# Performance work log

Measured on AMD Instinct MI355X. Metric: run time of the kernel, lower is better.

Reference implementation:

```python
import jax, jax.numpy as jnp
import numpy as np

B, N, C, HEADS = 8, 1024, 768, 12
HW = 32  # H = W = 32, so H*W == N


def _layernorm(x, g, b, eps=1e-5):
    mu = x.mean(-1, keepdims=True)
    var = ((x - mu) ** 2).mean(-1, keepdims=True)
    return (x - mu) * jax.lax.rsqrt(var + eps) * g + b


def setup_inputs() -> dict:
    key = jax.random.key(0)
    ks = jax.random.split(key, 6)
    w = lambda k, shape: jax.random.normal(k, shape, dtype=jnp.float32) * 0.02
    return {
        "x": jax.random.normal(ks[0], (B, N, C), dtype=jnp.float32),
        "y": jax.random.normal(ks[1], (B, C, HW, HW), dtype=jnp.float32),
        "q_w": w(ks[2], (C, C)),
        "q_b": jnp.zeros((C,), jnp.float32),
        "kv_w": w(ks[3], (2 * C, C)),
        "kv_b": jnp.zeros((2 * C,), jnp.float32),
        "proj_w": w(ks[4], (C, C)),
        "proj_b": jnp.zeros((C,), jnp.float32),
        "ln_g": jnp.ones((C,), jnp.float32),
        "ln_b": jnp.zeros((C,), jnp.float32),
        "H": HW,
        "W": HW,
    }


def reference(x, y, q_w, q_b, kv_w, kv_b, proj_w, proj_b, ln_g, ln_b, H, W):
    Bn, Nn, Cn = x.shape
    hd = Cn // HEADS
    scale = hd ** -0.5  # qk_scale=None, c_ratio=1 -> head_dim**-0.5

    # gating tensors from y
    y1 = y.reshape(Bn, Cn, H * W).transpose(0, 2, 1)          # [B, N, C]
    y2 = _layernorm(y1, ln_g, ln_b)
    yq = jax.nn.sigmoid(y2 @ q_w.T + q_b)                      # [B, N, C]
    ykv = jax.nn.sigmoid(y2 @ kv_w.T + kv_b)                   # [B, N, 2C]

    # gated q: q2 = q0 + q0*yq
    q0 = x @ q_w.T + q_b
    q = (q0 + q0 * yq).reshape(Bn, Nn, HEADS, hd).transpose(0, 2, 1, 3)  # [B,h,N,d]

    # gated kv: kv2 = kv0*ykv + ykv
    kv0 = x @ kv_w.T + kv_b
    kv = (kv0 * ykv + ykv).reshape(Bn, Nn, 2, HEADS, hd).transpose(2, 0, 3, 1, 4)
    k, v = kv[0], kv[1]                                        # [B,h,N,d] each

    attn = jax.nn.softmax(jnp.einsum("bhqd,bhkd->bhqk", q, k) * scale, axis=-1)
    out = jnp.einsum("bhqk,bhkd->bhqd", attn, v)
    out = out.transpose(0, 2, 1, 3).reshape(Bn, Nn, Cn)
    return out @ proj_w.T + proj_b
```

## Files before the change

### kernel.cpp

```cpp
#include <hip/hip_runtime.h>
#include <stdint.h>

typedef __attribute__((ext_vector_type(4))) float f4;
typedef __attribute__((ext_vector_type(8))) short bf16x8;
typedef __attribute__((ext_vector_type(4))) unsigned short u16x4;
typedef unsigned short u16;

#define B_ 8
#define N_ 1024
#define C_ 768
#define NH 12
#define HD 64

__device__ __forceinline__ float bf2f(u16 v) {
  union { unsigned u; float f; } x; x.u = ((unsigned)v) << 16; return x.f;
}
__device__ __forceinline__ u16 f2bf(float f) {
  union { float f; unsigned u; } x; x.f = f;
  unsigned r = x.u + 0x7FFFu + ((x.u >> 16) & 1u);
  return (u16)(r >> 16);
}
__device__ __forceinline__ void g2l16(const u16* g, const u16* l) {
  __builtin_amdgcn_global_load_lds(
      (const __attribute__((address_space(1))) void*)(uintptr_t)g,
      (__attribute__((address_space(3))) void*)(uint32_t)(uintptr_t)l,
      16, 0, 0);
}

#define SW12() asm volatile("s_waitcnt vmcnt(12)" ::: "memory")
#define SW6()  asm volatile("s_waitcnt vmcnt(6)" ::: "memory")
#define SW4()  asm volatile("s_waitcnt vmcnt(4)" ::: "memory")
#define SW3()  asm volatile("s_waitcnt vmcnt(3)" ::: "memory")
#define SW2()  asm volatile("s_waitcnt vmcnt(2)" ::: "memory")
#define SW0()  asm volatile("s_waitcnt vmcnt(0)" ::: "memory")
#define BARF()                              \
  do {                                      \
    __builtin_amdgcn_s_barrier();           \
    asm volatile("" ::: "memory");          \
    __builtin_amdgcn_sched_barrier(0);      \
  } while (0)

__global__ __launch_bounds__(256) void cvt_bf16(const float* __restrict__ s,
                                                u16* __restrict__ d, int n4) {
  int i = blockIdx.x * 256 + threadIdx.x;
  int stride = gridDim.x * 256;
  for (; i < n4; i += stride) {
    float4 v = ((const float4*)s)[i];
    u16x4 o;
    o.x = f2bf(v.x); o.y = f2bf(v.y); o.z = f2bf(v.z); o.w = f2bf(v.w);
    ((u16x4*)d)[i] = o;
  }
}

__global__ __launch_bounds__(512) void ln_fused(const float* __restrict__ y,
                                                const float* __restrict__ lg,
                                                const float* __restrict__ lb,
                                                u16* __restrict__ y2c,
                                                int b0) {
  __shared__ u16 ybuf[768 * 33];
  __shared__ float ps[16][32], pq[16][32];
  __shared__ float smu[32], srs[32];
  int t = threadIdx.x;
  int nl = t & 31, ch = t >> 5;
  int idx0 = b0 * N_ + blockIdx.x * 32;
  int b = idx0 >> 10, nb_ = idx0 & 1023;
  const float* p = y + (size_t)b * C_ * N_ + nb_ + nl;
  float s = 0.f, q = 0.f;
  int c0 = ch * 48;
  for (int c = c0; c < c0 + 48; ++c) {
    float v = p[(size_t)c * N_];
    s += v; q += v * v;
    ybuf[c * 33 + nl] = f2bf(v);
  }
  ps[ch][nl] = s; pq[ch][nl] = q;
  __syncthreads();
  if (t < 32) {
    float ts = 0.f, tq = 0.f;
    for (int g = 0; g < 16; ++g) { ts += ps[g][t]; tq += pq[g][t]; }
    float m = ts * (1.f / C_);
    float var = tq * (1.f / C_) - m * m;
    smu[t] = m;
    srs[t] = rsqrtf(fmaxf(var, 0.f) + 1e-5f);
  }
  __syncthreads();
  int rn = t >> 4, cg = t & 15;
  float m = smu[rn], rr = srs[rn];
  int bl = b - b0;
  int n = nb_ + rn;
  u16* dst = y2c + ((size_t)bl * N_ + n) * C_ + cg * 48;
  for (int cc = 0; cc < 48; cc += 8) {
    int c = cg * 48 + cc;
    bf16x8 o;
    for (int j = 0; j < 8; ++j) {
      float v = bf2f(ybuf[(c + j) * 33 + rn]);
      o[j] = (short)f2bf((v - m) * rr * lg[c + j] + lb[c + j]);
    }
    *(bf16x8*)(dst + cc) = o;
  }
}

__global__ __launch_bounds__(256, 2) void gemm_gate(
    const u16* __restrict__ xbc, const u16* __restrict__ y2c,
    const u16* __restrict__ qwb, const u16* __restrict__ kvwb,
    const float* __restrict__ qb_, const float* __restrict__ kvb_,
    u16* __restrict__ o_q, u16* __restrict__ o_k, u16* __restrict__ o_vT) {
  __shared__ u16 smem[36864];
  int t = threadIdx.x, l = t & 63;
  int quad = l >> 4, l15 = l & 15;
  int w = t >> 6, wm = w & 1, wn = w >> 1;
  int m0l = blockIdx.x * 128;
  int n0l = blockIdx.y * 128;

  const u16* wp; const float* bp; int sel, h0;
  if (n0l < C_) {
    wp = qwb + (size_t)n0l * C_; bp = qb_ + n0l; sel = 0; h0 = n0l >> 6;
  } else {
    int nk = n0l - C_;
    wp = kvwb + (size_t)nk * C_; bp = kvb_ + nk;
    sel = (nk < C_) ? 1 : 2;
    h0 = ((sel == 2) ? nk - C_ : nk) >> 6;
  }

  f4 accx[4][4], accy[4][4];
  for (int i = 0; i < 4; ++i)
    for (int j = 0; j < 4; ++j) {
      accx[i][j] = (f4){0.f, 0.f, 0.f, 0.f};
      accy[i][j] = (f4){0.f, 0.f, 0.f, 0.f};
    }

  int row = t >> 2;
  int colS = (((t & 3) ^ (row & 3)) * 8);
  const u16* gx = xbc + (size_t)(m0l + row) * C_ + colS;
  const u16* gy = y2c + (size_t)(m0l + row) * C_ + colS;
  const u16* gw = wp + (size_t)row * C_ + colS;
  int rsl = (quad ^ (l15 & 3)) * 8;

#define STAGE_G(OFF, kk)                                   \
  do {                                                     \
    u16* p_ = smem + (OFF);                                \
    g2l16(gx + (kk),           p_ + t * 8);                \
    g2l16(gx + (kk) + 64 * C_, p_ + 2048 + t * 8);         \
    g2l16(gy + (kk),           p_ + 4096 + t * 8);         \
    g2l16(gy + (kk) + 64 * C_, p_ + 6144 + t * 8);         \
    g2l16(gw + (kk),           p_ + 8192 + t * 8);         \
    g2l16(gw + (kk) + 64 * C_, p_ + 10240 + t * 8);        \
  } while (0)

#define COMPUTE_G(OFF)                                                        \
  do {                                                                        \
    const u16* base = smem + (OFF);                                           \
    bf16x8 afx[4], afy[4], bfr[4];                                            \
    for (int i = 0; i < 4; ++i) {                                             \
      int ra = (wm * 64 + i * 16 + l15) * 32 + rsl;                           \
      afx[i] = *(const bf16x8*)&base[ra];                                     \
      afy[i] = *(const bf16x8*)&base[4096 + ra];                              \
      int rb = (wn * 64 + i * 16 + l15) * 32 + rsl;                           \
      bfr[i] = *(const bf16x8*)&base[8192 + rb];                              \
    }                                                                         \
    for (int i = 0; i < 4; ++i)                                               \
      for (int j = 0; j < 4; ++j) {                                           \
        accx[i][j] = __builtin_amdgcn_mfma_f32_16x16x32_bf16(afx[i], bfr[j], accx[i][j], 0, 0, 0); \
        accy[i][j] = __builtin_amdgcn_mfma_f32_16x16x32_bf16(afy[i], bfr[j], accy[i][j], 0, 0, 0); \
      }                                                                       \
  } while (0)

#define STEP_G(i, OFF)                                        \
  do {                                                        \
    COMPUTE_G(OFF);                                           \
    BARF();                                                   \
    if ((i) < 21)      { STAGE_G(OFF, ((i) + 3) * 32); SW12(); } \
    else if ((i) == 21) SW6();                                \
    else if ((i) == 22) SW0();                                \
    BARF();                                                   \
  } while (0)

  STAGE_G(0, 0);
  STAGE_G(12288, 32);
  STAGE_G(24576, 64);
  SW12();
  BARF();
#pragma unroll
  for (int n = 0; n < 24; n += 3) {
    STEP_G(n, 0);
    STEP_G(n + 1, 12288);
    STEP_G(n + 2, 24576);
  }
#undef STEP_G
#undef STAGE_G
#undef COMPUTE_G

  const int PITCH = 136;
  for (int j = 0; j < 4; ++j) {
    int cloc = wn * 64 + j * 16 + l15;
    float bias = bp[cloc];
    for (int i = 0; i < 4; ++i) {
      int rb0 = wm * 64 + i * 16 + quad * 4;
      for (int r = 0; r < 4; ++r) {
        int rloc = rb0 + r;
        float vx = accx[i][j][r] + bias;
        float vy = accy[i][j][r] + bias;
        float gg = 1.f / (1.f + __expf(-vy));
        float val = (sel == 0) ? vx * (1.f + gg) : gg * (vx + 1.f);
        u16 bv = f2bf(val);
        if (sel == 2) smem[cloc * PITCH + rloc] = bv;
        else          smem[rloc * PITCH + cloc] = bv;
      }
    }
  }
  __syncthreads();
  {
    int rr = t >> 1, hh = t & 1;
    const u16* src = smem + rr * PITCH + hh * 64;
    u16* dst;
    if (sel == 2) {
      int h = h0 + (rr >> 6), d = rr & 63;
      int bl = m0l >> 10, nbase = m0l & 1023;
      dst = o_vT + (size_t)((bl * NH + h) * HD + d) * N_ + nbase + hh * 64;
    } else {
      int gml = m0l + rr;
      int bl = gml >> 10, n = gml & 1023;
      int h = h0 + hh;
      dst = (sel == 0 ? o_q : o_k) + (size_t)((bl * NH + h) * N_ + n) * HD;
    }
    for (int c = 0; c < 8; ++c) {
      bf16x8 v = *(const bf16x8*)(src + c * 8);
      *(bf16x8*)(dst + c * 8) = v;
    }
  }
}

__global__ __launch_bounds__(512) void attn(const u16* __restrict__ qoc,
                                            const u16* __restrict__ koc,
                                            const u16* __restrict__ vTc,
                                            u16* __restrict__ aoc) {
  __shared__ u16 Qs[8192], Ks[8192], Vs[8192];
  __shared__ u16 Ps[128 * 72];
  int t = threadIdx.x, l = t & 63, w = t >> 6;
  int quad = l >> 4, l15 = l & 15;
  int bhl = blockIdx.y;
  int bl = bhl / NH, h = bhl % NH;
  int q0 = blockIdx.x * 128;
  int sr = t >> 3;
  int swo = ((t & 7) ^ (sr & 7)) * 8;
  const u16* qbp = qoc + ((size_t)bhl * N_ + q0) * HD;
  const u16* kb = koc + (size_t)bhl * N_ * HD;
  const u16* vb = vTc + (size_t)bhl * HD * N_;

#define STAGE_KV(OFF, key0)                                                \
  do {                                                                     \
    g2l16(kb + (size_t)((key0) + sr) * HD + swo, Ks + (OFF) + t * 8);      \
    g2l16(vb + (size_t)sr * N_ + (key0) + swo,   Vs + (OFF) + t * 8);      \
  } while (0)

  g2l16(qbp + (size_t)sr * HD + swo,        Qs + t * 8);
  g2l16(qbp + (size_t)(64 + sr) * HD + swo, Qs + 4096 + t * 8);
  STAGE_KV(0, 0);
  STAGE_KV(4096, 64);
  SW2();
  BARF();

  int sA = (quad ^ (l15 & 7)) * 8;
  int sB = sA ^ 32;
  bf16x8 aq0 = *(const bf16x8*)&Qs[(w * 16 + l15) * 64 + sA];
  bf16x8 aq1 = *(const bf16x8*)&Qs[(w * 16 + l15) * 64 + sB];
  f4 o[4];
  for (int i = 0; i < 4; ++i) o[i] = (f4){0.f, 0.f, 0.f, 0.f};
  f4 ls = (f4){0.f, 0.f, 0.f, 0.f};
  bf16x8 ones;
  for (int i = 0; i < 8; ++i) ones[i] = (short)0x3F80;

#define TILE_STEP(KOFF)                                                       \
  do {                                                                        \
    f4 s_[4];                                                                 \
    __builtin_amdgcn_s_setprio(1);                                            \
    for (int ni = 0; ni < 4; ++ni) {                                          \
      bf16x8 b0v = *(const bf16x8*)&Ks[(KOFF) + (ni * 16 + l15) * 64 + sA];   \
      bf16x8 b1v = *(const bf16x8*)&Ks[(KOFF) + (ni * 16 + l15) * 64 + sB];   \
      f4 z = (f4){0.f, 0.f, 0.f, 0.f};                                        \
      z = __builtin_amdgcn_mfma_f32_16x16x32_bf16(aq0, b0v, z, 0, 0, 0);      \
      z = __builtin_amdgcn_mfma_f32_16x16x32_bf16(aq1, b1v, z, 0, 0, 0);      \
      s_[ni] = z;                                                             \
    }                                                                         \
    __builtin_amdgcn_s_setprio(0);                                            \
    for (int ni = 0; ni < 4; ++ni)                                            \
      for (int r = 0; r < 4; ++r)                                             \
        Ps[(w * 16 + quad * 4 + r) * 72 + ni * 16 + l15] =                    \
            f2bf(__expf(s_[ni][r] * 0.125f));                                 \
    bf16x8 ap0 = *(const bf16x8*)&Ps[(w * 16 + l15) * 72 + quad * 8];         \
    bf16x8 ap1 = *(const bf16x8*)&Ps[(w * 16 + l15) * 72 + 32 + quad * 8];    \
    __builtin_amdgcn_s_setprio(1);                                            \
    for (int ni = 0; ni < 4; ++ni) {                                          \
      bf16x8 b0v = *(const bf16x8*)&Vs[(KOFF) + (ni * 16 + l15) * 64 + sA];   \
      bf16x8 b1v = *(const bf16x8*)&Vs[(KOFF) + (ni * 16 + l15) * 64 + sB];   \
      o[ni] = __builtin_amdgcn_mfma_f32_16x16x32_bf16(ap0, b0v, o[ni], 0, 0, 0); \
      o[ni] = __builtin_amdgcn_mfma_f32_16x16x32_bf16(ap1, b1v, o[ni], 0, 0, 0); \
    }                                                                         \
    ls = __builtin_amdgcn_mfma_f32_16x16x32_bf16(ap0, ones, ls, 0, 0, 0);     \
    ls = __builtin_amdgcn_mfma_f32_16x16x32_bf16(ap1, ones, ls, 0, 0, 0);     \
    __builtin_amdgcn_s_setprio(0);                                            \
  } while (0)

  for (int kt = 0; kt < 16; kt += 2) {
    TILE_STEP(0);
    BARF();
    if (kt + 2 < 16) { STAGE_KV(0, (kt + 2) * 64); SW2(); } else { SW0(); }
    BARF();
    TILE_STEP(4096);
    BARF();
    if (kt + 3 < 16) { STAGE_KV(4096, (kt + 3) * 64); SW2(); } else { SW0(); }
    BARF();
  }
#undef TILE_STEP
#undef STAGE_KV

  for (int ni = 0; ni < 4; ++ni)
    for (int r = 0; r < 4; ++r)
      Ps[(w * 16 + quad * 4 + r) * 72 + ni * 16 + l15] =
          f2bf(o[ni][r] / ls[r]);
  __syncthreads();
  {
    int rr = t >> 2, cc = t & 3;
    int n = q0 + rr;
    const u16* src = Ps + rr * 72 + cc * 16;
    u16* dst = aoc + ((size_t)bl * N_ + n) * C_ + h * HD + cc * 16;
    *(bf16x8*)dst = *(const bf16x8*)src;
    *(bf16x8*)(dst + 8) = *(const bf16x8*)(src + 8);
  }
}

__global__ __launch_bounds__(256, 2) void gemm_proj(const u16* __restrict__ aoc,
                                                    const u16* __restrict__ pwb,
                                                    const float* __restrict__ bias,
                                                    float* __restrict__ out,
                                                    int b0) {
  __shared__ u16 smem[24576];
  int t = threadIdx.x, l = t & 63;
  int quad = l >> 4, l15 = l & 15;
  int w = t >> 6, wm = w & 1, wn = w >> 1;
  int m0l = blockIdx.x * 128, n0 = blockIdx.y * 64;
  f4 acc[4][2];
  for (int i = 0; i < 4; ++i)
    for (int j = 0; j < 2; ++j) acc[i][j] = (f4){0.f, 0.f, 0.f, 0.f};
  int row = t >> 2, colb = (t & 3) * 8;
  const u16* ga = aoc + (size_t)(m0l + row) * C_ + colb;
  const u16* gw = pwb + (size_t)(n0 + row) * C_ + colb;

#define STAGE_P(OFF, kk)                                        \
  do {                                                          \
    u16* p_ = smem + (OFF);                                     \
    g2l16(ga + (kk),                p_ + t * 8);                \
    g2l16(ga + (kk) + 64 * C_,      p_ + 2048 + t * 8);         \
    g2l16(ga + (kk) + 32,           p_ + 4096 + t * 8);         \
    g2l16(ga + (kk) + 32 + 64 * C_, p_ + 6144 + t * 8);         \
    g2l16(gw + (kk),                p_ + 8192 + t * 8);         \
    g2l16(gw + (kk) + 32,           p_ + 10240 + t * 8);        \
  } while (0)

#define COMPUTE_P(OFF)                                                        \
  do {                                                                        \
    const u16* base = smem + (OFF);                                           \
    _Pragma("unroll")                                                         \
    for (int kh = 0; kh < 2; ++kh) {                                          \
      bf16x8 af[4], bfr[2];                                                   \
      for (int i = 0; i < 4; ++i)                                             \
        af[i] = *(const bf16x8*)&base[kh * 4096 + (wm * 64 + i * 16 + l15) * 32 + quad * 8]; \
      for (int j = 0; j < 2; ++j)                                             \
        bfr[j] = *(const bf16x8*)&base[8192 + kh * 2048 + (wn * 32 + j * 16 + l15) * 32 + quad * 8]; \
      for (int i = 0; i < 4; ++i)                                             \
        for (int j = 0; j < 2; ++j)                                           \
          acc[i][j] = __builtin_amdgcn_mfma_f32_16x16x32_bf16(af[i], bfr[j], acc[i][j], 0, 0, 0); \
    }                                                                         \
  } while (0)

  STAGE_P(0, 0);
  STAGE_P(12288, 64);
  SW6();
  BARF();
  for (int n = 0; n < 12; n += 2) {
    COMPUTE_P(0);
    BARF();
    if (n + 2 < 12) { STAGE_P(0, (n + 2) * 64); SW6(); } else { SW0(); }
    BARF();
    COMPUTE_P(12288);
    BARF();
    if (n + 3 < 12) { STAGE_P(12288, (n + 3) * 64); SW6(); } else { SW0(); }
    BARF();
  }
#undef STAGE_P
#undef COMPUTE_P

  for (int j = 0; j < 2; ++j) {
    int gcol = n0 + wn * 32 + j * 16 + l15;
    float bv = bias[gcol];
    for (int i = 0; i < 4; ++i) {
      int rbase = m0l + wm * 64 + i * 16 + quad * 4;
      for (int r = 0; r < 4; ++r)
        __builtin_nontemporal_store(acc[i][j][r] + bv,
                                    &out[(size_t)(b0 * N_ + rbase + r) * C_ + gcol]);
    }
  }
}

extern "C" void kernel_launch(void* const* d_in, const int* in_sizes, int n_in,
                              void* d_out, int out_size, void* d_ws, size_t ws_size,
                              hipStream_t stream) {
  const float* x   = (const float*)d_in[0];
  const float* y   = (const float*)d_in[1];
  const float* qw  = (const float*)d_in[2];
  const float* qb  = (const float*)d_in[3];
  const float* kvw = (const float*)d_in[4];
  const float* kvb = (const float*)d_in[5];
  const float* pw  = (const float*)d_in[6];
  const float* pb  = (const float*)d_in[7];
  const float* lg  = (const float*)d_in[8];
  const float* lb  = (const float*)d_in[9];

  char* ws = (char*)d_ws;
  u16* qwb  = (u16*)(ws + 65536);
  u16* kvwb = (u16*)(ws + 1245184);
  u16* pwb  = (u16*)(ws + 3604480);
  const size_t BASE2 = 4784128;
  const size_t PER_B = 1572864;

  int nb = 1;
  for (int c = 8; c >= 1; c >>= 1) {
    if (BASE2 + 5 * (size_t)c * PER_B <= ws_size) { nb = c; break; }
  }
  u16* xbc = (u16*)(ws + BASE2);
  u16* y2c = (u16*)(ws + BASE2 + (size_t)nb * PER_B);
  u16* qoc = (u16*)(ws + BASE2 + 2 * (size_t)nb * PER_B);
  u16* koc = (u16*)(ws + BASE2 + 3 * (size_t)nb * PER_B);
  u16* vTc = (u16*)(ws + BASE2 + 4 * (size_t)nb * PER_B);
  u16* aoc = xbc;

  cvt_bf16<<<dim3(576), dim3(256), 0, stream>>>(qw, qwb, 147456);
  cvt_bf16<<<dim3(1152), dim3(256), 0, stream>>>(kvw, kvwb, 294912);
  cvt_bf16<<<dim3(576), dim3(256), 0, stream>>>(pw, pwb, 147456);

  for (int b0 = 0; b0 < B_; b0 += nb) {
    cvt_bf16<<<dim3(768 * nb), dim3(256), 0, stream>>>(
        x + (size_t)b0 * N_ * C_, xbc, nb * 196608);
    ln_fused<<<dim3(32 * nb), dim3(512), 0, stream>>>(y, lg, lb, y2c, b0);
    gemm_gate<<<dim3(8 * nb, 18), dim3(256), 0, stream>>>(xbc, y2c, qwb, kvwb,
                                                          qb, kvb, qoc, koc, vTc);
    attn<<<dim3(8, 12 * nb), dim3(512), 0, stream>>>(qoc, koc, vTc, aoc);
    gemm_proj<<<dim3(8 * nb, 12), dim3(256), 0, stream>>>(aoc, pwb, pb, (float*)d_out, b0);
  }
}
```

Baseline: 268.2 us.

## Load K/V fragments directly from global memory, two query groups per wave

Replaces LDS-staged, double-buffered K/V tiles in the attention kernel with direct global-to-register fragment loads, and removes the block-wide barriers. Each wave now processes 32 query rows as two 16-row groups sharing each K/V fragment, and blocks shrink to 256 threads. This aims to cut LDS traffic and synchronisation overhead. In exchange, global loads are strided, less coalesced and not prefetched, so memory latency may be exposed.

```diff
diff --git a/kernel.cpp b/kernel.cpp
--- a/kernel.cpp
+++ b/kernel.cpp
@@ -29,9 +29,7 @@
 
 #define SW12() asm volatile("s_waitcnt vmcnt(12)" ::: "memory")
 #define SW6()  asm volatile("s_waitcnt vmcnt(6)" ::: "memory")
-#define SW4()  asm volatile("s_waitcnt vmcnt(4)" ::: "memory")
 #define SW3()  asm volatile("s_waitcnt vmcnt(3)" ::: "memory")
-#define SW2()  asm volatile("s_waitcnt vmcnt(2)" ::: "memory")
 #define SW0()  asm volatile("s_waitcnt vmcnt(0)" ::: "memory")
 #define BARF()                              \
   do {                                      \
@@ -229,102 +227,87 @@
   }
 }
 
-__global__ __launch_bounds__(512) void attn(const u16* __restrict__ qoc,
+__global__ __launch_bounds__(256) void attn(const u16* __restrict__ qoc,
                                             const u16* __restrict__ koc,
                                             const u16* __restrict__ vTc,
                                             u16* __restrict__ aoc) {
-  __shared__ u16 Qs[8192], Ks[8192], Vs[8192];
   __shared__ u16 Ps[128 * 72];
   int t = threadIdx.x, l = t & 63, w = t >> 6;
   int quad = l >> 4, l15 = l & 15;
   int bhl = blockIdx.y;
   int bl = bhl / NH, h = bhl % NH;
   int q0 = blockIdx.x * 128;
-  int sr = t >> 3;
-  int swo = ((t & 7) ^ (sr & 7)) * 8;
   const u16* qbp = qoc + ((size_t)bhl * N_ + q0) * HD;
   const u16* kb = koc + (size_t)bhl * N_ * HD;
   const u16* vb = vTc + (size_t)bhl * HD * N_;
 
-#define STAGE_KV(OFF, key0)                                                \
-  do {                                                                     \
-    g2l16(kb + (size_t)((key0) + sr) * HD + swo, Ks + (OFF) + t * 8);      \
-    g2l16(vb + (size_t)sr * N_ + (key0) + swo,   Vs + (OFF) + t * 8);      \
-  } while (0)
-
-  g2l16(qbp + (size_t)sr * HD + swo,        Qs + t * 8);
-  g2l16(qbp + (size_t)(64 + sr) * HD + swo, Qs + 4096 + t * 8);
-  STAGE_KV(0, 0);
-  STAGE_KV(4096, 64);
-  SW2();
-  BARF();
-
-  int sA = (quad ^ (l15 & 7)) * 8;
-  int sB = sA ^ 32;
-  bf16x8 aq0 = *(const bf16x8*)&Qs[(w * 16 + l15) * 64 + sA];
-  bf16x8 aq1 = *(const bf16x8*)&Qs[(w * 16 + l15) * 64 + sB];
-  f4 o[4];
-  for (int i = 0; i < 4; ++i) o[i] = (f4){0.f, 0.f, 0.f, 0.f};
-  f4 ls = (f4){0.f, 0.f, 0.f, 0.f};
+  bf16x8 aq[2][2];
+  for (int g = 0; g < 2; ++g) {
+    const u16* qrow = qbp + (size_t)(w * 32 + g * 16 + l15) * HD;
+    aq[g][0] = *(const bf16x8*)(qrow + quad * 8);
+    aq[g][1] = *(const bf16x8*)(qrow + 32 + quad * 8);
+  }
+
+  f4 o[2][4]; f4 ls[2];
+  for (int g = 0; g < 2; ++g) {
+    ls[g] = (f4){0.f, 0.f, 0.f, 0.f};
+    for (int i = 0; i < 4; ++i) o[g][i] = (f4){0.f, 0.f, 0.f, 0.f};
+  }
   bf16x8 ones;
   for (int i = 0; i < 8; ++i) ones[i] = (short)0x3F80;
 
-#define TILE_STEP(KOFF)                                                       \
-  do {                                                                        \
-    f4 s_[4];                                                                 \
-    __builtin_amdgcn_s_setprio(1);                                            \
-    for (int ni = 0; ni < 4; ++ni) {                                          \
-      bf16x8 b0v = *(const bf16x8*)&Ks[(KOFF) + (ni * 16 + l15) * 64 + sA];   \
-      bf16x8 b1v = *(const bf16x8*)&Ks[(KOFF) + (ni * 16 + l15) * 64 + sB];   \
-      f4 z = (f4){0.f, 0.f, 0.f, 0.f};                                        \
-      z = __builtin_amdgcn_mfma_f32_16x16x32_bf16(aq0, b0v, z, 0, 0, 0);      \
-      z = __builtin_amdgcn_mfma_f32_16x16x32_bf16(aq1, b1v, z, 0, 0, 0);      \
-      s_[ni] = z;                                                             \
-    }                                                                         \
-    __builtin_amdgcn_s_setprio(0);                                            \
-    for (int ni = 0; ni < 4; ++ni)                                            \
-      for (int r = 0; r < 4; ++r)                                             \
-        Ps[(w * 16 + quad * 4 + r) * 72 + ni * 16 + l15] =                    \
-            f2bf(__expf(s_[ni][r] * 0.125f));                                 \
-    bf16x8 ap0 = *(const bf16x8*)&Ps[(w * 16 + l15) * 72 + quad * 8];         \
-    bf16x8 ap1 = *(const bf16x8*)&Ps[(w * 16 + l15) * 72 + 32 + quad * 8];    \
-    __builtin_amdgcn_s_setprio(1);                                            \
-    for (int ni = 0; ni < 4; ++ni) {                                          \
-      bf16x8 b0v = *(const bf16x8*)&Vs[(KOFF) + (ni * 16 + l15) * 64 + sA];   \
-      bf16x8 b1v = *(const bf16x8*)&Vs[(KOFF) + (ni * 16 + l15) * 64 + sB];   \
-      o[ni] = __builtin_amdgcn_mfma_f32_16x16x32_bf16(ap0, b0v, o[ni], 0, 0, 0); \
-      o[ni] = __builtin_amdgcn_mfma_f32_16x16x32_bf16(ap1, b1v, o[ni], 0, 0, 0); \
-    }                                                                         \
-    ls = __builtin_amdgcn_mfma_f32_16x16x32_bf16(ap0, ones, ls, 0, 0, 0);     \
-    ls = __builtin_amdgcn_mfma_f32_16x16x32_bf16(ap1, ones, ls, 0, 0, 0);     \
-    __builtin_amdgcn_s_setprio(0);                                            \
-  } while (0)
-
-  for (int kt = 0; kt < 16; kt += 2) {
-    TILE_STEP(0);
-    BARF();
-    if (kt + 2 < 16) { STAGE_KV(0, (kt + 2) * 64); SW2(); } else { SW0(); }
-    BARF();
-    TILE_STEP(4096);
-    BARF();
-    if (kt + 3 < 16) { STAGE_KV(4096, (kt + 3) * 64); SW2(); } else { SW0(); }
-    BARF();
-  }
-#undef TILE_STEP
-#undef STAGE_KV
-
-  for (int ni = 0; ni < 4; ++ni)
-    for (int r = 0; r < 4; ++r)
-      Ps[(w * 16 + quad * 4 + r) * 72 + ni * 16 + l15] =
-          f2bf(o[ni][r] / ls[r]);
+  for (int kt = 0; kt < 16; ++kt) {
+    int key0 = kt * 64;
+    f4 s_[2][4];
+    for (int ni = 0; ni < 4; ++ni) {
+      const u16* krow = kb + (size_t)(key0 + ni * 16 + l15) * HD;
+      bf16x8 b0 = *(const bf16x8*)(krow + quad * 8);
+      bf16x8 b1 = *(const bf16x8*)(krow + 32 + quad * 8);
+      for (int g = 0; g < 2; ++g) {
+        f4 z = (f4){0.f, 0.f, 0.f, 0.f};
+        z = __builtin_amdgcn_mfma_f32_16x16x32_bf16(aq[g][0], b0, z, 0, 0, 0);
+        z = __builtin_amdgcn_mfma_f32_16x16x32_bf16(aq[g][1], b1, z, 0, 0, 0);
+        s_[g][ni] = z;
+      }
+    }
+    for (int g = 0; g < 2; ++g)
+      for (int ni = 0; ni < 4; ++ni)
+        for (int r = 0; r < 4; ++r)
+          Ps[(w * 32 + g * 16 + quad * 4 + r) * 72 + ni * 16 + l15] =
+              f2bf(__expf(s_[g][ni][r] * 0.125f));
+    bf16x8 ap[2][2];
+    for (int g = 0; g < 2; ++g) {
+      ap[g][0] = *(const bf16x8*)&Ps[(w * 32 + g * 16 + l15) * 72 + quad * 8];
+      ap[g][1] = *(const bf16x8*)&Ps[(w * 32 + g * 16 + l15) * 72 + 32 + quad * 8];
+    }
+    for (int ni = 0; ni < 4; ++ni) {
+      const u16* vrow = vb + (size_t)(ni * 16 + l15) * N_ + key0;
+      bf16x8 b0 = *(const bf16x8*)(vrow + quad * 8);
+      bf16x8 b1 = *(const bf16x8*)(vrow + 32 + quad * 8);
+      for (int g = 0; g < 2; ++g) {
+        o[g][ni] = __builtin_amdgcn_mfma_f32_16x16x32_bf16(ap[g][0], b0, o[g][ni], 0, 0, 0);
+        o[g][ni] = __builtin_amdgcn_mfma_f32_16x16x32_bf16(ap[g][1], b1, o[g][ni], 0, 0, 0);
+      }
+    }
+    for (int g = 0; g < 2; ++g) {
+      ls[g] = __builtin_amdgcn_mfma_f32_16x16x32_bf16(ap[g][0], ones, ls[g], 0, 0, 0);
+      ls[g] = __builtin_amdgcn_mfma_f32_16x16x32_bf16(ap[g][1], ones, ls[g], 0, 0, 0);
+    }
+  }
+
+  for (int g = 0; g < 2; ++g)
+    for (int ni = 0; ni < 4; ++ni)
+      for (int r = 0; r < 4; ++r)
+        Ps[(w * 32 + g * 16 + quad * 4 + r) * 72 + ni * 16 + l15] =
+            f2bf(o[g][ni][r] / ls[g][r]);
   __syncthreads();
   {
-    int rr = t >> 2, cc = t & 3;
+    int rr = t >> 1, cc = t & 1;
     int n = q0 + rr;
-    const u16* src = Ps + rr * 72 + cc * 16;
-    u16* dst = aoc + ((size_t)bl * N_ + n) * C_ + h * HD + cc * 16;
-    *(bf16x8*)dst = *(const bf16x8*)src;
-    *(bf16x8*)(dst + 8) = *(const bf16x8*)(src + 8);
+    const u16* src = Ps + rr * 72 + cc * 32;
+    u16* dst = aoc + ((size_t)bl * N_ + n) * C_ + h * HD + cc * 32;
+    for (int c = 0; c < 4; ++c)
+      *(bf16x8*)(dst + c * 8) = *(const bf16x8*)(src + c * 8);
   }
 }
 
@@ -443,7 +426,7 @@
     ln_fused<<<dim3(32 * nb), dim3(512), 0, stream>>>(y, lg, lb, y2c, b0);
     gemm_gate<<<dim3(8 * nb, 18), dim3(256), 0, stream>>>(xbc, y2c, qwb, kvwb,
                                                           qb, kvb, qoc, koc, vTc);
-    attn<<<dim3(8, 12 * nb), dim3(512), 0, stream>>>(qoc, koc, vTc, aoc);
+    attn<<<dim3(8, 12 * nb), dim3(256), 0, stream>>>(qoc, koc, vTc, aoc);
     gemm_proj<<<dim3(8 * nb, 12), dim3(256), 0, stream>>>(aoc, pwb, pb, (float*)d_out, b0);
   }
 }
```

New measurement: 319.0 us. +18.9%, slower.
